# Kernel optimization log

Measured on AMD Instinct MI355X. Metric: run time of the kernel, lower is better.

## Reference

```python
import jax, jax.numpy as jnp
import numpy as np

N = 65536
H = 512
E = 8
OUT = 2

def setup_inputs() -> dict:
    key = jax.random.key(0)
    ks = jax.random.split(key, 9)
    s = 0.1
    return {
        "x": jax.random.normal(ks[0], (N, 10), dtype=jnp.float32),
        "w1": jax.random.normal(ks[1], (H,), dtype=jnp.float32) * s,        # fc1: Linear(1,H) weight
        "b1": jax.random.normal(ks[2], (H,), dtype=jnp.float32) * s,
        "meta_w": jax.random.normal(ks[3], (E, H), dtype=jnp.float32) * s,  # 8 Linear(1,H) weights stacked
        "meta_b": jax.random.normal(ks[4], (E, H), dtype=jnp.float32) * s,
        "w2": jax.random.normal(ks[5], (H, H), dtype=jnp.float32) * s,      # fc2 weight (in,out layout)
        "b2": jax.random.normal(ks[6], (H,), dtype=jnp.float32) * s,
        "w3": jax.random.normal(ks[7], (H, OUT), dtype=jnp.float32) * s,    # fc3 weight
        "b3": jax.random.normal(ks[8], (OUT,), dtype=jnp.float32) * s,
    }

def reference(x, w1, b1, meta_w, meta_b, w2, b2, w3, b3):
    one_hot = x[:, 0:8]          # [N,8] expert combine weights
    delta = x[:, 8:9]            # [N,1]
    phi = x[:, 9:10]             # [N,1]
    # fc1(delta): Linear with input_dim=1 -> outer product with weight column
    x1 = delta * w1[None, :] + b1[None, :]                       # [N,H]
    # Per-expert Linear(1,H) on phi, combined with one_hot. Since each expert
    # is linear in phi, the dense [N,H,8] tensor + matmul of the original
    # collapses exactly to: phi * (one_hot @ meta_w) + one_hot @ meta_b.
    x2 = phi * (one_hot @ meta_w) + one_hot @ meta_b             # [N,H]
    h = jax.nn.relu(x1 + x2)
    h = jax.nn.relu(h @ w2 + b2)
    return h @ w3 + b3                                           # [N,OUT]
```

## Files before the change

### kernel.cpp

```cpp
#include <hip/hip_runtime.h>


#define BM 64

typedef float f32x4 __attribute__((ext_vector_type(4)));
typedef short s16x8 __attribute__((ext_vector_type(8)));

__device__ __forceinline__ short f2bf(float f) {
    union { float f; unsigned u; } c; c.f = f;
    unsigned u = c.u;
    return (short)((u + 0x7FFFu + ((u >> 16) & 1u)) >> 16);
}

__global__ void prep_kernel(const float* __restrict__ w1, const float* __restrict__ b1,
                            const float* __restrict__ mw, const float* __restrict__ mb,
                            const float* __restrict__ w2,
                            short* __restrict__ w2s, short* __restrict__ waugS) {
    int id = blockIdx.x * 256 + threadIdx.x;
    if (id < 512 * 512) {
        int k = id / 512, n = id % 512;
        int ks = k >> 5, g = (k >> 3) & 3, j = k & 7;
        w2s[(((ks * 4 + g) * 512) + n) * 8 + j] = f2bf(w2[id]);
    }
    if (id < 512 * 32) {
        int col = id >> 5, k = id & 31;
        float v = 0.f;
        if (k < 8)        v = mw[k * 512 + col];
        else if (k < 16)  v = mb[(k - 8) * 512 + col];
        else if (k == 16) v = w1[col];
        else if (k == 17) v = b1[col];
        waugS[col * 32 + k] = f2bf(v);
    }
}

__global__ __launch_bounds__(512, 4) void fused_mlp(
    const float* __restrict__ x, const short* __restrict__ waugS,
    const short* __restrict__ w2s, const float* __restrict__ b2,
    const float* __restrict__ w3, const float* __restrict__ b3,
    float* __restrict__ out) {

    __shared__ __align__(16) short haug[64 * 512];
    __shared__ float xls[64 * 10];
    __shared__ float oacc[128];

    const int tid  = threadIdx.x;
    const int wv   = tid >> 6;
    const int lane = tid & 63;
    const int l15  = lane & 15;
    const int g    = lane >> 4;
    const long rowbase = (long)blockIdx.x * BM;

    for (int i = tid; i < BM * 10; i += 512) xls[i] = x[rowbase * 10 + i];
    if (tid < 128) oacc[tid] = 0.f;
    __syncthreads();

    {
        s16x8 afr[4];
#pragma unroll
        for (int m = 0; m < 4; ++m) {
            int r = m * 16 + l15;
            float v[8];
            if (g == 0) {
                float phi = xls[r * 10 + 9];
#pragma unroll
                for (int j = 0; j < 8; ++j) v[j] = xls[r * 10 + j] * phi;
            } else if (g == 1) {
#pragma unroll
                for (int j = 0; j < 8; ++j) v[j] = xls[r * 10 + j];
            } else if (g == 2) {
                v[0] = xls[r * 10 + 8]; v[1] = 1.f;
#pragma unroll
                for (int j = 2; j < 8; ++j) v[j] = 0.f;
            } else {
#pragma unroll
                for (int j = 0; j < 8; ++j) v[j] = 0.f;
            }
            s16x8 a;
#pragma unroll
            for (int j = 0; j < 8; ++j) a[j] = f2bf(v[j]);
            afr[m] = a;
        }
#pragma unroll
        for (int nf = 0; nf < 4; ++nf) {
            int col = wv * 64 + nf * 16 + l15;
            s16x8 bfr = *(const s16x8*)(waugS + col * 32 + g * 8);
            int chi = (col >> 3) * 512 + (col & 7);
#pragma unroll
            for (int m = 0; m < 4; ++m) {
                f32x4 c = {0.f, 0.f, 0.f, 0.f};
                c = __builtin_amdgcn_mfma_f32_16x16x32_bf16(afr[m], bfr, c, 0, 0, 0);
#pragma unroll
                for (int r4 = 0; r4 < 4; ++r4) {
                    int row = m * 16 + g * 4 + r4;
                    float hv = c[r4];
                    hv = hv > 0.f ? hv : 0.f;
                    haug[chi + row * 8] = f2bf(hv);
                }
            }
        }
    }
    __syncthreads();

    f32x4 acc[4][4];
#pragma unroll
    for (int m = 0; m < 4; ++m)
#pragma unroll
        for (int n = 0; n < 4; ++n) acc[m][n] = (f32x4){0.f, 0.f, 0.f, 0.f};

    const char* hb = (const char*)haug + g * 1024 + l15 * 16;
    const s16x8* __restrict__ w2v = (const s16x8*)w2s;
    const int colbase = wv * 64 + l15;

    for (int t = 0; t < 16; ++t) {
        const s16x8* p = w2v + (t * 4 + g) * 512 + colbase;
        s16x8 bf[4];
#pragma unroll
        for (int n = 0; n < 4; ++n) bf[n] = p[n * 16];
        const char* hbt = hb + t * 4096;
        s16x8 af[4];
#pragma unroll
        for (int m = 0; m < 4; ++m)
            af[m] = *(const s16x8*)(hbt + m * 256);
#pragma unroll
        for (int m = 0; m < 4; ++m)
#pragma unroll
            for (int n = 0; n < 4; ++n)
                acc[m][n] = __builtin_amdgcn_mfma_f32_16x16x32_bf16(af[m], bf[n], acc[m][n], 0, 0, 0);
    }

    float bb2[4], w30[4], w31[4];
#pragma unroll
    for (int n = 0; n < 4; ++n) {
        int col = wv * 64 + n * 16 + l15;
        bb2[n] = b2[col];
        w30[n] = w3[col * 2 + 0];
        w31[n] = w3[col * 2 + 1];
    }
#pragma unroll
    for (int m = 0; m < 4; ++m) {
#pragma unroll
        for (int r4 = 0; r4 < 4; ++r4) {
            float s0 = 0.f, s1 = 0.f;
#pragma unroll
            for (int n = 0; n < 4; ++n) {
                float v = acc[m][n][r4] + bb2[n];
                v = v > 0.f ? v : 0.f;
                s0 += v * w30[n];
                s1 += v * w31[n];
            }
            s0 += __shfl_xor(s0, 1); s1 += __shfl_xor(s1, 1);
            s0 += __shfl_xor(s0, 2); s1 += __shfl_xor(s1, 2);
            s0 += __shfl_xor(s0, 4); s1 += __shfl_xor(s1, 4);
            s0 += __shfl_xor(s0, 8); s1 += __shfl_xor(s1, 8);
            if (l15 == 0) {
                int row = m * 16 + g * 4 + r4;
                atomicAdd(&oacc[row * 2 + 0], s0);
                atomicAdd(&oacc[row * 2 + 1], s1);
            }
        }
    }
    __syncthreads();

    if (tid < 128) {
        int row = tid >> 1, o = tid & 1;
        out[(rowbase + row) * 2 + o] = oacc[tid] + b3[o];
    }
}

extern "C" void kernel_launch(void* const* d_in, const int* in_sizes, int n_in,
                              void* d_out, int out_size, void* d_ws, size_t ws_size,
                              hipStream_t stream) {
    const float* x  = (const float*)d_in[0];
    const float* w1 = (const float*)d_in[1];
    const float* b1 = (const float*)d_in[2];
    const float* mw = (const float*)d_in[3];
    const float* mb = (const float*)d_in[4];
    const float* w2 = (const float*)d_in[5];
    const float* b2 = (const float*)d_in[6];
    const float* w3 = (const float*)d_in[7];
    const float* b3 = (const float*)d_in[8];
    float* out = (float*)d_out;

    short* w2s   = (short*)d_ws;
    short* waugS = w2s + 512 * 512;

    prep_kernel<<<1024, 256, 0, stream>>>(w1, b1, mw, mb, w2, w2s, waugS);
    fused_mlp<<<65536 / BM, 512, 0, stream>>>(x, waugS, w2s, b2, w3, b3, out);
}
```

Baseline: 55.96 us.

## Switch fc2 GEMM to 32x32x16 MFMA with matching W2 and LDS layout

Replaces the 4x4 grid of 16x16x32 bf16 MFMAs per wave with a 2x2 grid of 32x32x16 MFMAs, and repacks W2 into 8-element k-chunks to match the new operand layout. Larger MFMA tiles halve operand loads per FLOP (fewer LDS and global fragment reads) and reduce instruction count. The epilogue reduction is rewritten for the 32-lane row mapping with one extra shuffle stage. This risks more LDS bank conflicts on the A reads and a higher register count for the 16-wide accumulators.

```diff
diff --git a/kernel.cpp b/kernel.cpp
--- a/kernel.cpp
+++ b/kernel.cpp
@@ -3,8 +3,9 @@
 
 #define BM 64
 
-typedef float f32x4 __attribute__((ext_vector_type(4)));
-typedef short s16x8 __attribute__((ext_vector_type(8)));
+typedef float f32x4  __attribute__((ext_vector_type(4)));
+typedef float f32x16 __attribute__((ext_vector_type(16)));
+typedef short s16x8  __attribute__((ext_vector_type(8)));
 
 __device__ __forceinline__ short f2bf(float f) {
     union { float f; unsigned u; } c; c.f = f;
@@ -19,8 +20,7 @@
     int id = blockIdx.x * 256 + threadIdx.x;
     if (id < 512 * 512) {
         int k = id / 512, n = id % 512;
-        int ks = k >> 5, g = (k >> 3) & 3, j = k & 7;
-        w2s[(((ks * 4 + g) * 512) + n) * 8 + j] = f2bf(w2[id]);
+        w2s[((k >> 3) * 512 + n) * 8 + (k & 7)] = f2bf(w2[id]);
     }
     if (id < 512 * 32) {
         int col = id >> 5, k = id & 31;
@@ -48,6 +48,8 @@
     const int lane = tid & 63;
     const int l15  = lane & 15;
     const int g    = lane >> 4;
+    const int hi   = lane >> 5;
+    const int l31  = lane & 31;
     const long rowbase = (long)blockIdx.x * BM;
 
     for (int i = tid; i < BM * 10; i += 512) xls[i] = x[rowbase * 10 + i];
@@ -101,59 +103,56 @@
     }
     __syncthreads();
 
-    f32x4 acc[4][4];
+    f32x16 acc[2][2];
 #pragma unroll
-    for (int m = 0; m < 4; ++m)
+    for (int a = 0; a < 2; ++a)
 #pragma unroll
-        for (int n = 0; n < 4; ++n) acc[m][n] = (f32x4){0.f, 0.f, 0.f, 0.f};
+        for (int b = 0; b < 2; ++b)
+#pragma unroll
+            for (int e = 0; e < 16; ++e) acc[a][b][e] = 0.f;
 
-    const char* hb = (const char*)haug + g * 1024 + l15 * 16;
-    const s16x8* __restrict__ w2v = (const s16x8*)w2s;
-    const int colbase = wv * 64 + l15;
+    const char* habase = (const char*)haug + hi * 1024 + l31 * 16;
+    const s16x8* __restrict__ w2base = (const s16x8*)w2s + hi * 512 + wv * 64 + l31;
 
-    for (int t = 0; t < 16; ++t) {
-        const s16x8* p = w2v + (t * 4 + g) * 512 + colbase;
-        s16x8 bf[4];
-#pragma unroll
-        for (int n = 0; n < 4; ++n) bf[n] = p[n * 16];
-        const char* hbt = hb + t * 4096;
-        s16x8 af[4];
-#pragma unroll
-        for (int m = 0; m < 4; ++m)
-            af[m] = *(const s16x8*)(hbt + m * 256);
-#pragma unroll
-        for (int m = 0; m < 4; ++m)
-#pragma unroll
-            for (int n = 0; n < 4; ++n)
-                acc[m][n] = __builtin_amdgcn_mfma_f32_16x16x32_bf16(af[m], bf[n], acc[m][n], 0, 0, 0);
+#pragma unroll 4
+    for (int s = 0; s < 32; ++s) {
+        s16x8 b0 = w2base[s * 1024];
+        s16x8 b1 = w2base[s * 1024 + 32];
+        s16x8 a0 = *(const s16x8*)(habase + s * 2048);
+        s16x8 a1 = *(const s16x8*)(habase + s * 2048 + 512);
+        acc[0][0] = __builtin_amdgcn_mfma_f32_32x32x16_bf16(a0, b0, acc[0][0], 0, 0, 0);
+        acc[0][1] = __builtin_amdgcn_mfma_f32_32x32x16_bf16(a0, b1, acc[0][1], 0, 0, 0);
+        acc[1][0] = __builtin_amdgcn_mfma_f32_32x32x16_bf16(a1, b0, acc[1][0], 0, 0, 0);
+        acc[1][1] = __builtin_amdgcn_mfma_f32_32x32x16_bf16(a1, b1, acc[1][1], 0, 0, 0);
     }
 
-    float bb2[4], w30[4], w31[4];
+    float b2c[2], w30c[2], w31c[2];
 #pragma unroll
-    for (int n = 0; n < 4; ++n) {
-        int col = wv * 64 + n * 16 + l15;
-        bb2[n] = b2[col];
-        w30[n] = w3[col * 2 + 0];
-        w31[n] = w3[col * 2 + 1];
+    for (int cb = 0; cb < 2; ++cb) {
+        int c = wv * 64 + cb * 32 + l31;
+        b2c[cb] = b2[c];
+        w30c[cb] = w3[c * 2 + 0];
+        w31c[cb] = w3[c * 2 + 1];
     }
 #pragma unroll
-    for (int m = 0; m < 4; ++m) {
+    for (int mb = 0; mb < 2; ++mb) {
 #pragma unroll
-        for (int r4 = 0; r4 < 4; ++r4) {
+        for (int reg = 0; reg < 16; ++reg) {
             float s0 = 0.f, s1 = 0.f;
 #pragma unroll
-            for (int n = 0; n < 4; ++n) {
-                float v = acc[m][n][r4] + bb2[n];
+            for (int cb = 0; cb < 2; ++cb) {
+                float v = acc[mb][cb][reg] + b2c[cb];
                 v = v > 0.f ? v : 0.f;
-                s0 += v * w30[n];
-                s1 += v * w31[n];
+                s0 += v * w30c[cb];
+                s1 += v * w31c[cb];
             }
-            s0 += __shfl_xor(s0, 1); s1 += __shfl_xor(s1, 1);
-            s0 += __shfl_xor(s0, 2); s1 += __shfl_xor(s1, 2);
-            s0 += __shfl_xor(s0, 4); s1 += __shfl_xor(s1, 4);
-            s0 += __shfl_xor(s0, 8); s1 += __shfl_xor(s1, 8);
-            if (l15 == 0) {
-                int row = m * 16 + g * 4 + r4;
+            s0 += __shfl_xor(s0, 1);  s1 += __shfl_xor(s1, 1);
+            s0 += __shfl_xor(s0, 2);  s1 += __shfl_xor(s1, 2);
+            s0 += __shfl_xor(s0, 4);  s1 += __shfl_xor(s1, 4);
+            s0 += __shfl_xor(s0, 8);  s1 += __shfl_xor(s1, 8);
+            s0 += __shfl_xor(s0, 16); s1 += __shfl_xor(s1, 16);
+            if (l31 == 0) {
+                int row = mb * 32 + (reg & 3) + 8 * (reg >> 2) + 4 * hi;
                 atomicAdd(&oacc[row * 2 + 0], s0);
                 atomicAdd(&oacc[row * 2 + 1], s1);
             }
```

Result: slower. 70.08 us (+25.2%).

## Stream W2 tiles into LDS via async global_load_lds triple-buffered ring

Applied to the files above, without the earlier changes.

Replaces direct global loads of W2 B-fragments in the main MFMA loop with per-wave asynchronous global->LDS copies into a 3-stage ring, issued ahead of use with manual vmcnt/lgkmcnt waits and a fully unrolled 16-step loop. The aim is to hide global load latency behind MFMA work. LDS use grows to 160KB per block and the occupancy hint is dropped, so only one block fits per CU, and xls/oacc now alias ring memory, so oacc is zeroed later behind extra barriers.

```diff
diff --git a/kernel.cpp b/kernel.cpp
--- a/kernel.cpp
+++ b/kernel.cpp
@@ -10,6 +10,12 @@
     union { float f; unsigned u; } c; c.f = f;
     unsigned u = c.u;
     return (short)((u + 0x7FFFu + ((u >> 16) & 1u)) >> 16);
+}
+
+__device__ __forceinline__ void gload16(const void* g, void* l) {
+    __builtin_amdgcn_global_load_lds(
+        (const __attribute__((address_space(1))) void*)g,
+        (__attribute__((address_space(3))) void*)l, 16, 0, 0);
 }
 
 __global__ void prep_kernel(const float* __restrict__ w1, const float* __restrict__ b1,
@@ -33,15 +39,15 @@
     }
 }
 
-__global__ __launch_bounds__(512, 4) void fused_mlp(
+__global__ __launch_bounds__(512) void fused_mlp(
     const float* __restrict__ x, const short* __restrict__ waugS,
     const short* __restrict__ w2s, const float* __restrict__ b2,
     const float* __restrict__ w3, const float* __restrict__ b3,
     float* __restrict__ out) {
 
-    __shared__ __align__(16) short haug[64 * 512];
-    __shared__ float xls[64 * 10];
-    __shared__ float oacc[128];
+    __shared__ __align__(16) char Lall[163840];
+    short* haug = (short*)Lall;
+    char*  ring = Lall + 65536;
 
     const int tid  = threadIdx.x;
     const int wv   = tid >> 6;
@@ -50,8 +56,26 @@
     const int g    = lane >> 4;
     const long rowbase = (long)blockIdx.x * BM;
 
+    float* xls  = (float*)(ring + 2 * 4096);
+    float* oacc = (float*)(ring + 2 * 4096 + 2560);
+
+    char* ringw = ring + wv * 12288;
+    const char* srcp = (const char*)w2s + g * 8192 + wv * 1024 + l15 * 16;
+
+#define STAGE4(T, S)                                         \
+    do {                                                     \
+        const char* s_ = srcp + (size_t)(T) * 32768;         \
+        char* d_ = ringw + (S) * 4096;                       \
+        gload16(s_,       d_);                               \
+        gload16(s_ + 256, d_ + 1024);                        \
+        gload16(s_ + 512, d_ + 2048);                        \
+        gload16(s_ + 768, d_ + 3072);                        \
+    } while (0)
+
+    STAGE4(0, 0);
+    STAGE4(1, 1);
+
     for (int i = tid; i < BM * 10; i += 512) xls[i] = x[rowbase * 10 + i];
-    if (tid < 128) oacc[tid] = 0.f;
     __syncthreads();
 
     {
@@ -101,32 +125,76 @@
     }
     __syncthreads();
 
+    STAGE4(2, 2);
+
     f32x4 acc[4][4];
 #pragma unroll
     for (int m = 0; m < 4; ++m)
 #pragma unroll
         for (int n = 0; n < 4; ++n) acc[m][n] = (f32x4){0.f, 0.f, 0.f, 0.f};
 
-    const char* hb = (const char*)haug + g * 1024 + l15 * 16;
-    const s16x8* __restrict__ w2v = (const s16x8*)w2s;
-    const int colbase = wv * 64 + l15;
-
-    for (int t = 0; t < 16; ++t) {
-        const s16x8* p = w2v + (t * 4 + g) * 512 + colbase;
-        s16x8 bf[4];
-#pragma unroll
-        for (int n = 0; n < 4; ++n) bf[n] = p[n * 16];
-        const char* hbt = hb + t * 4096;
-        s16x8 af[4];
-#pragma unroll
-        for (int m = 0; m < 4; ++m)
-            af[m] = *(const s16x8*)(hbt + m * 256);
-#pragma unroll
-        for (int m = 0; m < 4; ++m)
-#pragma unroll
-            for (int n = 0; n < 4; ++n)
-                acc[m][n] = __builtin_amdgcn_mfma_f32_16x16x32_bf16(af[m], bf[n], acc[m][n], 0, 0, 0);
-    }
+    const char* hbp = (const char*)haug + g * 1024 + l15 * 16;
+    const char* rbl = ringw + (size_t)lane * 16;
+
+#define WAITV8 do { asm volatile("s_waitcnt vmcnt(8)" ::: "memory"); __builtin_amdgcn_sched_barrier(0); } while (0)
+#define WAITV4 do { asm volatile("s_waitcnt vmcnt(4)" ::: "memory"); __builtin_amdgcn_sched_barrier(0); } while (0)
+#define WAITV0 do { asm volatile("s_waitcnt vmcnt(0)" ::: "memory"); __builtin_amdgcn_sched_barrier(0); } while (0)
+#define LGKM4  do { asm volatile("s_waitcnt lgkmcnt(4)" ::: "memory"); __builtin_amdgcn_sched_barrier(0); } while (0)
+
+#define ITER(T, S, DOSTAGE)                                                                  \
+    do {                                                                                     \
+        s16x8 b0 = *(const s16x8*)(rbl + (S) * 4096);                                        \
+        s16x8 b1 = *(const s16x8*)(rbl + (S) * 4096 + 1024);                                 \
+        s16x8 b2v = *(const s16x8*)(rbl + (S) * 4096 + 2048);                                \
+        s16x8 b3v = *(const s16x8*)(rbl + (S) * 4096 + 3072);                                \
+        __builtin_amdgcn_sched_barrier(0);                                                   \
+        s16x8 a0 = *(const s16x8*)(hbp + (T) * 4096);                                        \
+        s16x8 a1 = *(const s16x8*)(hbp + (T) * 4096 + 256);                                  \
+        s16x8 a2 = *(const s16x8*)(hbp + (T) * 4096 + 512);                                  \
+        s16x8 a3 = *(const s16x8*)(hbp + (T) * 4096 + 768);                                  \
+        LGKM4;                \
+        if (DOSTAGE) STAGE4((T) + 3, S);                                                     \
+        acc[0][0] = __builtin_amdgcn_mfma_f32_16x16x32_bf16(a0, b0,  acc[0][0], 0, 0, 0);    \
+        acc[0][1] = __builtin_amdgcn_mfma_f32_16x16x32_bf16(a0, b1,  acc[0][1], 0, 0, 0);    \
+        acc[0][2] = __builtin_amdgcn_mfma_f32_16x16x32_bf16(a0, b2v, acc[0][2], 0, 0, 0);    \
+        acc[0][3] = __builtin_amdgcn_mfma_f32_16x16x32_bf16(a0, b3v, acc[0][3], 0, 0, 0);    \
+        acc[1][0] = __builtin_amdgcn_mfma_f32_16x16x32_bf16(a1, b0,  acc[1][0], 0, 0, 0);    \
+        acc[1][1] = __builtin_amdgcn_mfma_f32_16x16x32_bf16(a1, b1,  acc[1][1], 0, 0, 0);    \
+        acc[1][2] = __builtin_amdgcn_mfma_f32_16x16x32_bf16(a1, b2v, acc[1][2], 0, 0, 0);    \
+        acc[1][3] = __builtin_amdgcn_mfma_f32_16x16x32_bf16(a1, b3v, acc[1][3], 0, 0, 0);    \
+        acc[2][0] = __builtin_amdgcn_mfma_f32_16x16x32_bf16(a2, b0,  acc[2][0], 0, 0, 0);    \
+        acc[2][1] = __builtin_amdgcn_mfma_f32_16x16x32_bf16(a2, b1,  acc[2][1], 0, 0, 0);    \
+        acc[2][2] = __builtin_amdgcn_mfma_f32_16x16x32_bf16(a2, b2v, acc[2][2], 0, 0, 0);    \
+        acc[2][3] = __builtin_amdgcn_mfma_f32_16x16x32_bf16(a2, b3v, acc[2][3], 0, 0, 0);    \
+        acc[3][0] = __builtin_amdgcn_mfma_f32_16x16x32_bf16(a3, b0,  acc[3][0], 0, 0, 0);    \
+        acc[3][1] = __builtin_amdgcn_mfma_f32_16x16x32_bf16(a3, b1,  acc[3][1], 0, 0, 0);    \
+        acc[3][2] = __builtin_amdgcn_mfma_f32_16x16x32_bf16(a3, b2v, acc[3][2], 0, 0, 0);    \
+        acc[3][3] = __builtin_amdgcn_mfma_f32_16x16x32_bf16(a3, b3v, acc[3][3], 0, 0, 0);    \
+    } while (0)
+
+    WAITV8; ITER(0, 0, 1);
+    WAITV8; ITER(1, 1, 1);
+    WAITV8; ITER(2, 2, 1);
+    WAITV8; ITER(3, 0, 1);
+    WAITV8; ITER(4, 1, 1);
+    WAITV8; ITER(5, 2, 1);
+    WAITV8; ITER(6, 0, 1);
+    WAITV8; ITER(7, 1, 1);
+    WAITV8; ITER(8, 2, 1);
+    WAITV8; ITER(9, 0, 1);
+    WAITV8; ITER(10, 1, 1);
+    WAITV8; ITER(11, 2, 1);
+    WAITV8; ITER(12, 0, 1);
+    WAITV8; ITER(13, 1, 0);
+    WAITV4; ITER(14, 2, 0);
+    WAITV0; ITER(15, 0, 0);
+
+#undef ITER
+#undef STAGE4
+
+    __syncthreads();
+    if (tid < 128) oacc[tid] = 0.f;
+    __syncthreads();
 
     float bb2[4], w30[4], w31[4];
 #pragma unroll
```

Result: slower. 69.43 us (+24.1%).

## Stage W2 tiles into LDS with async triple-buffered global_load_lds pipeline

Applied to the files above, without the earlier changes.

Replaces per-wave direct global loads of W2 fragments in the second GEMM with a triple-buffered pipeline. Each 32KB K-slice is copied straight into LDS with global_load_lds, two slices ahead of use, and consumed after an explicit vmcnt wait plus a barrier. MFMA sections are raised in priority, and the x and output-accumulator scratch are aliased onto the staging buffers. The aim is to hide global/L2 latency for the weights. In exchange, LDS use grows to 160KB per block, which cuts occupancy to one block per CU, and a workgroup barrier is added every iteration.

```diff
diff --git a/kernel.cpp b/kernel.cpp
--- a/kernel.cpp
+++ b/kernel.cpp
@@ -10,6 +10,12 @@
     union { float f; unsigned u; } c; c.f = f;
     unsigned u = c.u;
     return (short)((u + 0x7FFFu + ((u >> 16) & 1u)) >> 16);
+}
+
+__device__ __forceinline__ void gload16(const void* g, void* l) {
+    __builtin_amdgcn_global_load_lds(
+        (const __attribute__((address_space(1))) void*)g,
+        (__attribute__((address_space(3))) void*)l, 16, 0, 0);
 }
 
 __global__ void prep_kernel(const float* __restrict__ w1, const float* __restrict__ b1,
@@ -33,15 +39,15 @@
     }
 }
 
-__global__ __launch_bounds__(512, 4) void fused_mlp(
+__global__ __launch_bounds__(512) void fused_mlp(
     const float* __restrict__ x, const short* __restrict__ waugS,
     const short* __restrict__ w2s, const float* __restrict__ b2,
     const float* __restrict__ w3, const float* __restrict__ b3,
     float* __restrict__ out) {
 
-    __shared__ __align__(16) short haug[64 * 512];
-    __shared__ float xls[64 * 10];
-    __shared__ float oacc[128];
+    __shared__ __align__(16) char Lall[163840];
+    short* haug = (short*)Lall;
+    char*  bufs = Lall + 65536;
 
     const int tid  = threadIdx.x;
     const int wv   = tid >> 6;
@@ -50,8 +56,27 @@
     const int g    = lane >> 4;
     const long rowbase = (long)blockIdx.x * BM;
 
+    float* xls  = (float*)(bufs + 2 * 32768);
+    float* oacc = (float*)(bufs);
+
+    const char* srcS = (const char*)w2s + wv * 4096 + lane * 16;
+    char* dst0 = bufs + 0 * 32768 + wv * 4096;
+    char* dst1 = bufs + 1 * 32768 + wv * 4096;
+    char* dst2 = bufs + 2 * 32768 + wv * 4096;
+
+#define STAGE(T, DST)                                        \
+    do {                                                     \
+        const char* s_ = srcS + (size_t)(T) * 32768;         \
+        gload16(s_,        (DST));                           \
+        gload16(s_ + 1024, (DST) + 1024);                    \
+        gload16(s_ + 2048, (DST) + 2048);                    \
+        gload16(s_ + 3072, (DST) + 3072);                    \
+    } while (0)
+
+    STAGE(0, dst0);
+    STAGE(1, dst1);
+
     for (int i = tid; i < BM * 10; i += 512) xls[i] = x[rowbase * 10 + i];
-    if (tid < 128) oacc[tid] = 0.f;
     __syncthreads();
 
     {
@@ -107,26 +132,70 @@
 #pragma unroll
         for (int n = 0; n < 4; ++n) acc[m][n] = (f32x4){0.f, 0.f, 0.f, 0.f};
 
-    const char* hb = (const char*)haug + g * 1024 + l15 * 16;
-    const s16x8* __restrict__ w2v = (const s16x8*)w2s;
-    const int colbase = wv * 64 + l15;
-
-    for (int t = 0; t < 16; ++t) {
-        const s16x8* p = w2v + (t * 4 + g) * 512 + colbase;
-        s16x8 bf[4];
-#pragma unroll
-        for (int n = 0; n < 4; ++n) bf[n] = p[n * 16];
-        const char* hbt = hb + t * 4096;
-        s16x8 af[4];
-#pragma unroll
-        for (int m = 0; m < 4; ++m)
-            af[m] = *(const s16x8*)(hbt + m * 256);
-#pragma unroll
-        for (int m = 0; m < 4; ++m)
-#pragma unroll
-            for (int n = 0; n < 4; ++n)
-                acc[m][n] = __builtin_amdgcn_mfma_f32_16x16x32_bf16(af[m], bf[n], acc[m][n], 0, 0, 0);
-    }
+    const char* hb  = (const char*)haug + g * 1024 + l15 * 16;
+    const char* bp0 = bufs + 0 * 32768 + g * 8192 + (wv * 64 + l15) * 16;
+    const char* bp1 = bufs + 1 * 32768 + g * 8192 + (wv * 64 + l15) * 16;
+    const char* bp2 = bufs + 2 * 32768 + g * 8192 + (wv * 64 + l15) * 16;
+
+#define ITER(T, BP, DSTN, DOSTAGE, WN)                                                       \
+    do {                                                                                     \
+        asm volatile("s_waitcnt vmcnt(" WN ")" ::: "memory");                                \
+        __builtin_amdgcn_sched_barrier(0);                                                   \
+        __builtin_amdgcn_s_barrier();         \
+        s16x8 bq0 = *(const s16x8*)((BP));                                                   \
+        s16x8 bq1 = *(const s16x8*)((BP) + 256);                                             \
+        s16x8 bq2 = *(const s16x8*)((BP) + 512);                                             \
+        s16x8 bq3 = *(const s16x8*)((BP) + 768);                                             \
+        s16x8 aq0 = *(const s16x8*)(hb + (T) * 4096);                                        \
+        s16x8 aq1 = *(const s16x8*)(hb + (T) * 4096 + 256);                                  \
+        s16x8 aq2 = *(const s16x8*)(hb + (T) * 4096 + 512);                                  \
+        s16x8 aq3 = *(const s16x8*)(hb + (T) * 4096 + 768);                                  \
+        if (DOSTAGE) STAGE((T) + 2, DSTN);                  \
+        asm volatile("s_waitcnt lgkmcnt(0)" ::: "memory");                                   \
+        __builtin_amdgcn_sched_barrier(0);                                                   \
+        __builtin_amdgcn_s_setprio(1);                                                       \
+        acc[0][0] = __builtin_amdgcn_mfma_f32_16x16x32_bf16(aq0, bq0, acc[0][0], 0, 0, 0);   \
+        acc[0][1] = __builtin_amdgcn_mfma_f32_16x16x32_bf16(aq0, bq1, acc[0][1], 0, 0, 0);   \
+        acc[0][2] = __builtin_amdgcn_mfma_f32_16x16x32_bf16(aq0, bq2, acc[0][2], 0, 0, 0);   \
+        acc[0][3] = __builtin_amdgcn_mfma_f32_16x16x32_bf16(aq0, bq3, acc[0][3], 0, 0, 0);   \
+        acc[1][0] = __builtin_amdgcn_mfma_f32_16x16x32_bf16(aq1, bq0, acc[1][0], 0, 0, 0);   \
+        acc[1][1] = __builtin_amdgcn_mfma_f32_16x16x32_bf16(aq1, bq1, acc[1][1], 0, 0, 0);   \
+        acc[1][2] = __builtin_amdgcn_mfma_f32_16x16x32_bf16(aq1, bq2, acc[1][2], 0, 0, 0);   \
+        acc[1][3] = __builtin_amdgcn_mfma_f32_16x16x32_bf16(aq1, bq3, acc[1][3], 0, 0, 0);   \
+        acc[2][0] = __builtin_amdgcn_mfma_f32_16x16x32_bf16(aq2, bq0, acc[2][0], 0, 0, 0);   \
+        acc[2][1] = __builtin_amdgcn_mfma_f32_16x16x32_bf16(aq2, bq1, acc[2][1], 0, 0, 0);   \
+        acc[2][2] = __builtin_amdgcn_mfma_f32_16x16x32_bf16(aq2, bq2, acc[2][2], 0, 0, 0);   \
+        acc[2][3] = __builtin_amdgcn_mfma_f32_16x16x32_bf16(aq2, bq3, acc[2][3], 0, 0, 0);   \
+        acc[3][0] = __builtin_amdgcn_mfma_f32_16x16x32_bf16(aq3, bq0, acc[3][0], 0, 0, 0);   \
+        acc[3][1] = __builtin_amdgcn_mfma_f32_16x16x32_bf16(aq3, bq1, acc[3][1], 0, 0, 0);   \
+        acc[3][2] = __builtin_amdgcn_mfma_f32_16x16x32_bf16(aq3, bq2, acc[3][2], 0, 0, 0);   \
+        acc[3][3] = __builtin_amdgcn_mfma_f32_16x16x32_bf16(aq3, bq3, acc[3][3], 0, 0, 0);   \
+        __builtin_amdgcn_s_setprio(0);                                                       \
+    } while (0)
+
+    ITER(0,  bp0, dst2, 1, "4");
+    ITER(1,  bp1, dst0, 1, "4");
+    ITER(2,  bp2, dst1, 1, "4");
+    ITER(3,  bp0, dst2, 1, "4");
+    ITER(4,  bp1, dst0, 1, "4");
+    ITER(5,  bp2, dst1, 1, "4");
+    ITER(6,  bp0, dst2, 1, "4");
+    ITER(7,  bp1, dst0, 1, "4");
+    ITER(8,  bp2, dst1, 1, "4");
+    ITER(9,  bp0, dst2, 1, "4");
+    ITER(10, bp1, dst0, 1, "4");
+    ITER(11, bp2, dst1, 1, "4");
+    ITER(12, bp0, dst2, 1, "4");
+    ITER(13, bp1, dst0, 1, "4");
+    ITER(14, bp2, dst2, 0, "4");
+    ITER(15, bp0, dst0, 0, "0");
+
+#undef ITER
+#undef STAGE
+
+    __syncthreads();
+    if (tid < 128) oacc[tid] = 0.f;
+    __syncthreads();
 
     float bb2[4], w30[4], w31[4];
 #pragma unroll
```

Measured after the change: 68.88 us. +23.1%, slower.
